# Kernel tuning notes

Measured on AMD Instinct MI355X. Metric: run time of the kernel, lower is better.

The kernel has to match this reference:

```python
import jax, jax.numpy as jnp
from jax import lax
import numpy as np

B, L, D = 16, 512, 256
F, K = 256, 3
M = 2048
EPS = 1e-5


def setup_inputs() -> dict:
    key = jax.random.key(0)
    ks = jax.random.split(key, 12)
    x = jax.random.normal(ks[0], (B, L, D), jnp.float32)
    # integer durations >= 1, sum over L <= 3*512 = 1536 < M, as in training targets
    target = jax.random.randint(ks[1], (B, L), 1, 4)
    s = 0.02
    conv1_w = jax.random.normal(ks[2], (F, D, K), jnp.float32) * s
    conv1_b = jnp.zeros((F,), jnp.float32)
    ln1_g = jnp.ones((F,), jnp.float32)
    ln1_b = jnp.zeros((F,), jnp.float32)
    conv2_w = jax.random.normal(ks[3], (F, F, K), jnp.float32) * s
    conv2_b = jnp.zeros((F,), jnp.float32)
    ln2_g = jnp.ones((F,), jnp.float32)
    ln2_b = jnp.zeros((F,), jnp.float32)
    lin_w = jax.random.normal(ks[4], (F, 1), jnp.float32) * s
    lin_b = jnp.zeros((1,), jnp.float32)
    return dict(x=x, target=target, mel_max_length=M,
                conv1_w=conv1_w, conv1_b=conv1_b, ln1_g=ln1_g, ln1_b=ln1_b,
                conv2_w=conv2_w, conv2_b=conv2_b, ln2_g=ln2_g, ln2_b=ln2_b,
                lin_w=lin_w, lin_b=lin_b)


def _layer_norm(h, g, b):
    mu = jnp.mean(h, axis=-1, keepdims=True)
    var = jnp.mean(jnp.square(h - mu), axis=-1, keepdims=True)
    return (h - mu) * lax.rsqrt(var + EPS) * g + b


def _conv1d(h_bld, w, b):
    # h: (B, L, C_in), w: (C_out, C_in, K) -> (B, L, C_out), SAME padding
    pad = (w.shape[-1] - 1) // 2
    h = jnp.transpose(h_bld, (0, 2, 1))  # (B, C, L)
    h = lax.conv_general_dilated(h, w, (1,), [(pad, pad)],
                                 dimension_numbers=('NCH', 'OIH', 'NCH'))
    return jnp.transpose(h + b[None, :, None], (0, 2, 1))


def _duration_predictor(x, conv1_w, conv1_b, ln1_g, ln1_b,
                        conv2_w, conv2_b, ln2_g, ln2_b, lin_w, lin_b):
    # FastSpeech duration predictor (eval mode: dropout = identity)
    h = jax.nn.relu(_layer_norm(_conv1d(x, conv1_w, conv1_b), ln1_g, ln1_b))
    h = jax.nn.relu(_layer_norm(_conv1d(h, conv2_w, conv2_b), ln2_g, ln2_b))
    return jax.nn.relu(h @ lin_w + lin_b)[..., 0]  # (B, L)


def _length_regulate(x, dur, mel_max_length):
    # alignment[b,m,l] = 1 iff cs[l-1] <= m < cs[l]  (exactly the scatter+diff trick
    # of create_alignment, padded to mel_max_length as in the original F.pad)
    cs = jnp.cumsum(dur, axis=1)              # (B, L) inclusive cumsum
    prev = cs - dur                           # exclusive cumsum
    m = jnp.arange(mel_max_length)[None, :, None]  # (1, M, 1)
    align = ((m >= prev[:, None, :]) & (m < cs[:, None, :])).astype(x.dtype)  # (B,M,L)
    return jnp.einsum('bml,bld->bmd', align, x)


def reference(x, target, mel_max_length, conv1_w, conv1_b, ln1_g, ln1_b,
              conv2_w, conv2_b, ln2_g, ln2_b, lin_w, lin_b):
    dup = _duration_predictor(x, conv1_w, conv1_b, ln1_g, ln1_b,
                              conv2_w, conv2_b, ln2_g, ln2_b, lin_w, lin_b)
    output = _length_regulate(x, target, mel_max_length)
    return (output, dup)
```

## Files before the change

### kernel.cpp

```cpp
#include <hip/hip_runtime.h>
#include <hip/hip_bf16.h>

#define Bn 16
#define Ln 512
#define Cn 256
#define Fn 256
#define Kn 3
#define Mn 2048

#define NKSTEP 24
#define MT 32
#define XS_PS 264
#define NCONVBLK 256

typedef __attribute__((ext_vector_type(8))) short short8;
typedef __attribute__((ext_vector_type(4))) float f32x4;

static __device__ __forceinline__ unsigned short f2bf(float f) {
    unsigned int u = __float_as_uint(f);
    return (unsigned short)((u + 0x7fff + ((u >> 16) & 1)) >> 16);
}

__global__ __launch_bounds__(256) void pack_scan(
    const float* __restrict__ w1, const float* __restrict__ w2,
    unsigned short* __restrict__ bp1, unsigned short* __restrict__ bp2,
    const int* __restrict__ target, int* __restrict__ map)
{
    __shared__ int ss[256];
    const int blk = blockIdx.x;
    const int t = threadIdx.x;
    if (blk < 1536) {
        int i = blk * 256 + t;
        const float* w = w1;
        unsigned short* bp = bp1;
        if (i >= Fn * Cn * Kn) { i -= Fn * Cn * Kn; w = w2; bp = bp2; }
        int j    = i & 7;
        int lane = (i >> 3) & 63;
        int nt   = (i >> 9) & 15;
        int s    = i >> 13;
        int kap = s * 32 + ((lane >> 4) * 8) + j;
        int k = kap >> 8;
        int d = kap & 255;
        int f = nt * 16 + (lane & 15);
        bp[i] = f2bf(w[(f * Cn + d) * Kn + k]);
    } else {
        int b = blk - 1536;
        int v0 = target[b * Ln + 2 * t];
        int v1 = target[b * Ln + 2 * t + 1];
        ss[t] = v0 + v1;
        __syncthreads();
        for (int off = 1; off < 256; off <<= 1) {
            int add = (t >= off) ? ss[t - off] : 0;
            __syncthreads();
            ss[t] += add;
            __syncthreads();
        }
        int S     = ss[t];
        int total = ss[255];
        int cs1   = S;
        int cs0   = S - v1;
        int prev0 = cs0 - v0;
        for (int m = prev0; m < cs0; ++m) map[b * Mn + m] = 2 * t;
        for (int m = cs0;   m < cs1; ++m) map[b * Mn + m] = 2 * t + 1;
        for (int m = total + t; m < Mn; m += 256) map[b * Mn + m] = -1;
    }
}

template <bool IS_F32_IN, bool DO_LINEAR, bool WITH_REG>
__global__ __launch_bounds__(256) void conv_mfma(
    const void* __restrict__ in_,
    const unsigned short* __restrict__ bp,
    const float* __restrict__ bias,
    const float* __restrict__ gamma,
    const float* __restrict__ beta,
    const float* __restrict__ lw,
    const float* __restrict__ lb,
    unsigned short* __restrict__ hout,
    float* __restrict__ dup,
    const float* __restrict__ gx,
    const int* __restrict__ gmap,
    float* __restrict__ gout)
{
    __shared__ __align__(16) unsigned short xs[(MT + 2) * XS_PS];
    __shared__ float2 red[MT][4];
    __shared__ float  red2[MT][4];

    const int t = threadIdx.x;

    if (WITH_REG && blockIdx.x >= NCONVBLK) {
        int e4 = (blockIdx.x - NCONVBLK) * 256 + t;
        int d4 = e4 & 63;
        int bm = e4 >> 6;
        int b  = bm >> 11;
        int l  = gmap[bm];
        float4 val = make_float4(0.f, 0.f, 0.f, 0.f);
        if (l >= 0) val = *((const float4*)(gx + (size_t)(b * Ln + l) * Cn) + d4);
        ((float4*)gout)[e4] = val;
        return;
    }

    const int b  = blockIdx.x >> 4;
    const int l0 = (blockIdx.x & 15) * MT;

    if (IS_F32_IN) {
        const float* in = (const float*)in_;
        for (int idx = t; idx < (MT + 2) * 64; idx += 256) {
            int row = idx >> 6;
            int c4  = (idx & 63) * 4;
            int l = l0 + row - 1;
            float4 v = make_float4(0.f, 0.f, 0.f, 0.f);
            if (l >= 0 && l < Ln) v = *(const float4*)&in[((size_t)b * Ln + l) * Cn + c4];
            unsigned int lo = (unsigned int)f2bf(v.x) | ((unsigned int)f2bf(v.y) << 16);
            unsigned int hi = (unsigned int)f2bf(v.z) | ((unsigned int)f2bf(v.w) << 16);
            *(uint2*)&xs[row * XS_PS + c4] = make_uint2(lo, hi);
        }
    } else {
        const unsigned short* in = (const unsigned short*)in_;
        for (int idx = t; idx < (MT + 2) * 32; idx += 256) {
            int row = idx >> 5;
            int c8  = (idx & 31) * 8;
            int l = l0 + row - 1;
            uint4 v = make_uint4(0u, 0u, 0u, 0u);
            if (l >= 0 && l < Ln) v = *(const uint4*)&in[((size_t)b * Ln + l) * Cn + c8];
            *(uint4*)&xs[row * XS_PS + c8] = v;
        }
    }
    __syncthreads();

    const int lane = t & 63;
    const int wv   = t >> 6;
    const int mrow = lane & 15;
    const int q    = lane >> 4;

    f32x4  acc[2][4] = {};
    short8 bfr[2][4];
    short8 afr[2][2];

    auto loadB = [&](int s, int slot) {
        const unsigned short* p = bp + (size_t)((s * 16 + wv * 4) * 64 + lane) * 8;
        #pragma unroll
        for (int i = 0; i < 4; ++i)
            bfr[slot][i] = *(const short8*)(p + (size_t)i * 64 * 8);
    };
    auto loadA = [&](int s, int slot) {
        const int k    = s >> 3;
        const int dcol = (s & 7) * 32 + q * 8;
        #pragma unroll
        for (int mt = 0; mt < 2; ++mt)
            afr[slot][mt] = *(const short8*)&xs[(mt * 16 + mrow + k) * XS_PS + dcol];
    };

    loadB(0, 0); loadA(0, 0);
    loadB(1, 1); loadA(1, 1);

    #pragma unroll 2
    for (int s = 0; s < NKSTEP; ++s) {
        const int slot = s & 1;
        #pragma unroll
        for (int mt = 0; mt < 2; ++mt)
            #pragma unroll
            for (int i = 0; i < 4; ++i)
                acc[mt][i] = __builtin_amdgcn_mfma_f32_16x16x32_bf16(
                    afr[slot][mt], bfr[slot][i], acc[mt][i], 0, 0, 0);
        const int sn = (s + 2 < NKSTEP) ? (s + 2) : s;
        loadB(sn, slot);
        loadA(sn, slot);
    }

    float gv[4], bv[4], lwv[4], biasv[4];
    #pragma unroll
    for (int i = 0; i < 4; ++i) {
        int col = wv * 64 + i * 16 + mrow;
        biasv[i] = bias[col];
        gv[i]    = gamma[col];
        bv[i]    = beta[col];
        if (DO_LINEAR) lwv[i] = lw[col];
    }
    #pragma unroll
    for (int mt = 0; mt < 2; ++mt)
        #pragma unroll
        for (int i = 0; i < 4; ++i)
            #pragma unroll
            for (int r = 0; r < 4; ++r)
                acc[mt][i][r] += biasv[i];

    #pragma unroll
    for (int mt = 0; mt < 2; ++mt)
        #pragma unroll
        for (int r = 0; r < 4; ++r) {
            float s  = acc[mt][0][r] + acc[mt][1][r] + acc[mt][2][r] + acc[mt][3][r];
            float sq = acc[mt][0][r] * acc[mt][0][r] + acc[mt][1][r] * acc[mt][1][r]
                     + acc[mt][2][r] * acc[mt][2][r] + acc[mt][3][r] * acc[mt][3][r];
            #pragma unroll
            for (int off = 1; off <= 8; off <<= 1) {
                s  += __shfl_xor(s,  off, 64);
                sq += __shfl_xor(sq, off, 64);
            }
            if (mrow == 0) red[mt * 16 + q * 4 + r][wv] = make_float2(s, sq);
        }
    __syncthreads();

    float muv[2][4], rsv[2][4];
    #pragma unroll
    for (int mt = 0; mt < 2; ++mt)
        #pragma unroll
        for (int r = 0; r < 4; ++r) {
            int row = mt * 16 + q * 4 + r;
            float2 p0 = red[row][0], p1 = red[row][1], p2 = red[row][2], p3 = red[row][3];
            float s  = p0.x + p1.x + p2.x + p3.x;
            float sq = p0.y + p1.y + p2.y + p3.y;
            float mu  = s * (1.f / 256.f);
            float var = sq * (1.f / 256.f) - mu * mu;
            muv[mt][r] = mu;
            rsv[mt][r] = rsqrtf(var + 1e-5f);
        }

    if (!DO_LINEAR) {
        #pragma unroll
        for (int mt = 0; mt < 2; ++mt)
            #pragma unroll
            for (int r = 0; r < 4; ++r) {
                int l = l0 + mt * 16 + q * 4 + r;
                size_t base = ((size_t)b * Ln + l) * Fn;
                #pragma unroll
                for (int i = 0; i < 4; ++i) {
                    float o = fmaxf((acc[mt][i][r] - muv[mt][r]) * rsv[mt][r] * gv[i] + bv[i], 0.f);
                    hout[base + wv * 64 + i * 16 + mrow] = f2bf(o);
                }
            }
    } else {
        #pragma unroll
        for (int mt = 0; mt < 2; ++mt)
            #pragma unroll
            for (int r = 0; r < 4; ++r) {
                float dot = 0.f;
                #pragma unroll
                for (int i = 0; i < 4; ++i) {
                    float o = fmaxf((acc[mt][i][r] - muv[mt][r]) * rsv[mt][r] * gv[i] + bv[i], 0.f);
                    dot += o * lwv[i];
                }
                #pragma unroll
                for (int off = 1; off <= 8; off <<= 1)
                    dot += __shfl_xor(dot, off, 64);
                if (mrow == 0) red2[mt * 16 + q * 4 + r][wv] = dot;
            }
        __syncthreads();
        if (t < MT) {
            float d = red2[t][0] + red2[t][1] + red2[t][2] + red2[t][3];
            dup[b * Ln + l0 + t] = fmaxf(d + lb[0], 0.f);
        }
    }
}

extern "C" void kernel_launch(void* const* d_in, const int* in_sizes, int n_in,
                              void* d_out, int out_size, void* d_ws, size_t ws_size,
                              hipStream_t stream) {
    const float* x    = (const float*)d_in[0];
    const int*   targ = (const int*)d_in[1];
    const float* c1w = (const float*)d_in[3];
    const float* c1b = (const float*)d_in[4];
    const float* g1  = (const float*)d_in[5];
    const float* be1 = (const float*)d_in[6];
    const float* c2w = (const float*)d_in[7];
    const float* c2b = (const float*)d_in[8];
    const float* g2  = (const float*)d_in[9];
    const float* be2 = (const float*)d_in[10];
    const float* lw  = (const float*)d_in[11];
    const float* lb  = (const float*)d_in[12];

    float* out     = (float*)d_out;
    float* out_dup = out + (size_t)Bn * Mn * Cn;

    char* ws = (char*)d_ws;
    unsigned short* bp1 = (unsigned short*)ws;
    unsigned short* bp2 = (unsigned short*)(ws + 393216);
    unsigned short* h1  = (unsigned short*)(ws + 2 * 393216);
    int*            map = (int*)(ws + 2 * 393216 + 4194304);

    pack_scan<<<1552, 256, 0, stream>>>(c1w, c2w, bp1, bp2, targ, map);

    conv_mfma<true, false, true><<<NCONVBLK + (Bn * Mn * Cn / 4) / 256, 256, 0, stream>>>(
        (const void*)x, bp1, c1b, g1, be1, nullptr, nullptr, h1, nullptr,
        x, map, out);

    conv_mfma<false, true, false><<<NCONVBLK, 256, 0, stream>>>(
        (const void*)h1, bp2, c2b, g2, be2, lw, lb, nullptr, out_dup,
        nullptr, nullptr, nullptr);
}
```

Measured before the change: 117.8 us.

## Retile conv to 64-row tiles with 512 threads and move conv2 weight packing into gather kernel

Measured after the change: 141.9 us. 1.2x slower.

```diff
diff --git a/kernel.cpp b/kernel.cpp
--- a/kernel.cpp
+++ b/kernel.cpp
@@ -9,9 +9,11 @@
 #define Mn 2048
 
 #define NKSTEP 24
-#define MT 32
+#define MT 64
 #define XS_PS 264
-#define NCONVBLK 256
+#define NCONV 128
+#define NGATH 1024
+#define NPACK 384
 
 typedef __attribute__((ext_vector_type(8))) short short8;
 typedef __attribute__((ext_vector_type(4))) float f32x4;
@@ -21,53 +23,47 @@
     return (unsigned short)((u + 0x7fff + ((u >> 16) & 1)) >> 16);
 }
 
-__global__ __launch_bounds__(256) void pack_scan(
-    const float* __restrict__ w1, const float* __restrict__ w2,
-    unsigned short* __restrict__ bp1, unsigned short* __restrict__ bp2,
+static __device__ __forceinline__ void pack_one(const float* __restrict__ w,
+                                                unsigned short* __restrict__ bp,
+                                                int i) {
+    int j    = i & 7;
+    int lane = (i >> 3) & 63;
+    int nt   = (i >> 9) & 15;
+    int s    = i >> 13;
+    int kap = s * 32 + ((lane >> 4) * 8) + j;
+    int k = kap >> 8;
+    int d = kap & 255;
+    int f = nt * 16 + (lane & 15);
+    bp[i] = f2bf(w[(f * Cn + d) * Kn + k]);
+}
+
+__global__ __launch_bounds__(512) void pack_scan(
+    const float* __restrict__ w1, unsigned short* __restrict__ bp1,
     const int* __restrict__ target, int* __restrict__ map)
 {
-    __shared__ int ss[256];
+    __shared__ int ss[Ln];
     const int blk = blockIdx.x;
     const int t = threadIdx.x;
-    if (blk < 1536) {
-        int i = blk * 256 + t;
-        const float* w = w1;
-        unsigned short* bp = bp1;
-        if (i >= Fn * Cn * Kn) { i -= Fn * Cn * Kn; w = w2; bp = bp2; }
-        int j    = i & 7;
-        int lane = (i >> 3) & 63;
-        int nt   = (i >> 9) & 15;
-        int s    = i >> 13;
-        int kap = s * 32 + ((lane >> 4) * 8) + j;
-        int k = kap >> 8;
-        int d = kap & 255;
-        int f = nt * 16 + (lane & 15);
-        bp[i] = f2bf(w[(f * Cn + d) * Kn + k]);
-    } else {
-        int b = blk - 1536;
-        int v0 = target[b * Ln + 2 * t];
-        int v1 = target[b * Ln + 2 * t + 1];
-        ss[t] = v0 + v1;
+    if (blk < NPACK) { pack_one(w1, bp1, blk * 512 + t); return; }
+    int b = blk - NPACK;
+    int v = target[b * Ln + t];
+    ss[t] = v;
+    __syncthreads();
+    for (int off = 1; off < Ln; off <<= 1) {
+        int add = (t >= off) ? ss[t - off] : 0;
         __syncthreads();
-        for (int off = 1; off < 256; off <<= 1) {
-            int add = (t >= off) ? ss[t - off] : 0;
-            __syncthreads();
-            ss[t] += add;
-            __syncthreads();
-        }
-        int S     = ss[t];
-        int total = ss[255];
-        int cs1   = S;
-        int cs0   = S - v1;
-        int prev0 = cs0 - v0;
-        for (int m = prev0; m < cs0; ++m) map[b * Mn + m] = 2 * t;
-        for (int m = cs0;   m < cs1; ++m) map[b * Mn + m] = 2 * t + 1;
-        for (int m = total + t; m < Mn; m += 256) map[b * Mn + m] = -1;
-    }
-}
-
-template <bool IS_F32_IN, bool DO_LINEAR, bool WITH_REG>
-__global__ __launch_bounds__(256) void conv_mfma(
+        ss[t] += add;
+        __syncthreads();
+    }
+    int cs    = ss[t];
+    int prev  = cs - v;
+    int total = ss[Ln - 1];
+    for (int m = prev; m < cs; ++m) map[b * Mn + m] = t;
+    for (int m = total + t; m < Mn; m += Ln) map[b * Mn + m] = -1;
+}
+
+template <bool IS_F32_IN, bool DO_LINEAR, bool WITH_AUX>
+__global__ __launch_bounds__(512) void conv_mfma(
     const void* __restrict__ in_,
     const unsigned short* __restrict__ bp,
     const float* __restrict__ bias,
@@ -79,32 +75,41 @@
     float* __restrict__ dup,
     const float* __restrict__ gx,
     const int* __restrict__ gmap,
-    float* __restrict__ gout)
+    float* __restrict__ gout,
+    const float* __restrict__ wsrc,
+    unsigned short* __restrict__ bpdst)
 {
     __shared__ __align__(16) unsigned short xs[(MT + 2) * XS_PS];
-    __shared__ float2 red[MT][4];
-    __shared__ float  red2[MT][4];
+    __shared__ float2 red[MT][8];
+    __shared__ float  red2[MT][8];
 
     const int t = threadIdx.x;
 
-    if (WITH_REG && blockIdx.x >= NCONVBLK) {
-        int e4 = (blockIdx.x - NCONVBLK) * 256 + t;
-        int d4 = e4 & 63;
-        int bm = e4 >> 6;
-        int b  = bm >> 11;
-        int l  = gmap[bm];
-        float4 val = make_float4(0.f, 0.f, 0.f, 0.f);
-        if (l >= 0) val = *((const float4*)(gx + (size_t)(b * Ln + l) * Cn) + d4);
-        ((float4*)gout)[e4] = val;
+    if (WITH_AUX && blockIdx.x >= NCONV) {
+        int rel = blockIdx.x - NCONV;
+        if (rel < NGATH) {
+            int bm = rel * 32 + (t >> 4);
+            int l  = gmap[bm];
+            int b  = bm >> 11;
+            int lc = (l >= 0) ? l : 0;
+            const float4* src = (const float4*)(gx + ((size_t)b * Ln + lc) * Cn) + (t & 15);
+            float4* dst = (float4*)gout + (size_t)bm * 64 + (t & 15);
+            float4 z = make_float4(0.f, 0.f, 0.f, 0.f);
+            #pragma unroll
+            for (int j = 0; j < 4; ++j)
+                dst[j * 16] = (l >= 0) ? src[j * 16] : z;
+        } else {
+            pack_one(wsrc, bpdst, (rel - NGATH) * 512 + t);
+        }
         return;
     }
 
-    const int b  = blockIdx.x >> 4;
-    const int l0 = (blockIdx.x & 15) * MT;
+    const int b  = blockIdx.x >> 3;
+    const int l0 = (blockIdx.x & 7) * MT;
 
     if (IS_F32_IN) {
         const float* in = (const float*)in_;
-        for (int idx = t; idx < (MT + 2) * 64; idx += 256) {
+        for (int idx = t; idx < (MT + 2) * 64; idx += 512) {
             int row = idx >> 6;
             int c4  = (idx & 63) * 4;
             int l = l0 + row - 1;
@@ -116,7 +121,7 @@
         }
     } else {
         const unsigned short* in = (const unsigned short*)in_;
-        for (int idx = t; idx < (MT + 2) * 32; idx += 256) {
+        for (int idx = t; idx < (MT + 2) * 32; idx += 512) {
             int row = idx >> 5;
             int c8  = (idx & 31) * 8;
             int l = l0 + row - 1;
@@ -132,65 +137,62 @@
     const int mrow = lane & 15;
     const int q    = lane >> 4;
 
-    f32x4  acc[2][4] = {};
-    short8 bfr[2][4];
-    short8 afr[2][2];
+    f32x4  acc[4][2] = {};
+    short8 bfr[3][2];
+    short8 afr[3][4];
 
     auto loadB = [&](int s, int slot) {
-        const unsigned short* p = bp + (size_t)((s * 16 + wv * 4) * 64 + lane) * 8;
-        #pragma unroll
-        for (int i = 0; i < 4; ++i)
-            bfr[slot][i] = *(const short8*)(p + (size_t)i * 64 * 8);
+        const unsigned short* p = bp + (size_t)((s * 16 + wv * 2) * 64 + lane) * 8;
+        bfr[slot][0] = *(const short8*)p;
+        bfr[slot][1] = *(const short8*)(p + 512);
     };
     auto loadA = [&](int s, int slot) {
         const int k    = s >> 3;
         const int dcol = (s & 7) * 32 + q * 8;
         #pragma unroll
-        for (int mt = 0; mt < 2; ++mt)
+        for (int mt = 0; mt < 4; ++mt)
             afr[slot][mt] = *(const short8*)&xs[(mt * 16 + mrow + k) * XS_PS + dcol];
     };
 
     loadB(0, 0); loadA(0, 0);
     loadB(1, 1); loadA(1, 1);
-
-    #pragma unroll 2
+    loadB(2, 2); loadA(2, 2);
+
+    #pragma unroll
     for (int s = 0; s < NKSTEP; ++s) {
-        const int slot = s & 1;
-        #pragma unroll
-        for (int mt = 0; mt < 2; ++mt)
-            #pragma unroll
-            for (int i = 0; i < 4; ++i)
+        const int slot = s % 3;
+        #pragma unroll
+        for (int mt = 0; mt < 4; ++mt)
+            #pragma unroll
+            for (int i = 0; i < 2; ++i)
                 acc[mt][i] = __builtin_amdgcn_mfma_f32_16x16x32_bf16(
                     afr[slot][mt], bfr[slot][i], acc[mt][i], 0, 0, 0);
-        const int sn = (s + 2 < NKSTEP) ? (s + 2) : s;
-        loadB(sn, slot);
-        loadA(sn, slot);
-    }
-
-    float gv[4], bv[4], lwv[4], biasv[4];
-    #pragma unroll
-    for (int i = 0; i < 4; ++i) {
-        int col = wv * 64 + i * 16 + mrow;
+        if (s + 3 < NKSTEP) { loadB(s + 3, slot); loadA(s + 3, slot); }
+    }
+
+    float biasv[2], gv[2], bv[2], lwv[2];
+    #pragma unroll
+    for (int i = 0; i < 2; ++i) {
+        int col = wv * 32 + i * 16 + mrow;
         biasv[i] = bias[col];
         gv[i]    = gamma[col];
         bv[i]    = beta[col];
         if (DO_LINEAR) lwv[i] = lw[col];
     }
     #pragma unroll
-    for (int mt = 0; mt < 2; ++mt)
-        #pragma unroll
-        for (int i = 0; i < 4; ++i)
+    for (int mt = 0; mt < 4; ++mt)
+        #pragma unroll
+        for (int i = 0; i < 2; ++i)
             #pragma unroll
             for (int r = 0; r < 4; ++r)
                 acc[mt][i][r] += biasv[i];
 
     #pragma unroll
-    for (int mt = 0; mt < 2; ++mt)
+    for (int mt = 0; mt < 4; ++mt)
         #pragma unroll
         for (int r = 0; r < 4; ++r) {
-            float s  = acc[mt][0][r] + acc[mt][1][r] + acc[mt][2][r] + acc[mt][3][r];
-            float sq = acc[mt][0][r] * acc[mt][0][r] + acc[mt][1][r] * acc[mt][1][r]
-                     + acc[mt][2][r] * acc[mt][2][r] + acc[mt][3][r] * acc[mt][3][r];
+            float s  = acc[mt][0][r] + acc[mt][1][r];
+            float sq = acc[mt][0][r] * acc[mt][0][r] + acc[mt][1][r] * acc[mt][1][r];
             #pragma unroll
             for (int off = 1; off <= 8; off <<= 1) {
                 s  += __shfl_xor(s,  off, 64);
@@ -200,15 +202,18 @@
         }
     __syncthreads();
 
-    float muv[2][4], rsv[2][4];
-    #pragma unroll
-    for (int mt = 0; mt < 2; ++mt)
+    float muv[4][4], rsv[4][4];
+    #pragma unroll
+    for (int mt = 0; mt < 4; ++mt)
         #pragma unroll
         for (int r = 0; r < 4; ++r) {
             int row = mt * 16 + q * 4 + r;
-            float2 p0 = red[row][0], p1 = red[row][1], p2 = red[row][2], p3 = red[row][3];
-            float s  = p0.x + p1.x + p2.x + p3.x;
-            float sq = p0.y + p1.y + p2.y + p3.y;
+            float s = 0.f, sq = 0.f;
+            #pragma unroll
+            for (int w = 0; w < 8; ++w) {
+                float2 p = red[row][w];
+                s += p.x; sq += p.y;
+            }
             float mu  = s * (1.f / 256.f);
             float var = sq * (1.f / 256.f) - mu * mu;
             muv[mt][r] = mu;
@@ -217,25 +222,25 @@
 
     if (!DO_LINEAR) {
         #pragma unroll
-        for (int mt = 0; mt < 2; ++mt)
+        for (int mt = 0; mt < 4; ++mt)
             #pragma unroll
             for (int r = 0; r < 4; ++r) {
                 int l = l0 + mt * 16 + q * 4 + r;
                 size_t base = ((size_t)b * Ln + l) * Fn;
                 #pragma unroll
-                for (int i = 0; i < 4; ++i) {
+                for (int i = 0; i < 2; ++i) {
                     float o = fmaxf((acc[mt][i][r] - muv[mt][r]) * rsv[mt][r] * gv[i] + bv[i], 0.f);
-                    hout[base + wv * 64 + i * 16 + mrow] = f2bf(o);
+                    hout[base + wv * 32 + i * 16 + mrow] = f2bf(o);
                 }
             }
     } else {
         #pragma unroll
-        for (int mt = 0; mt < 2; ++mt)
+        for (int mt = 0; mt < 4; ++mt)
             #pragma unroll
             for (int r = 0; r < 4; ++r) {
                 float dot = 0.f;
                 #pragma unroll
-                for (int i = 0; i < 4; ++i) {
+                for (int i = 0; i < 2; ++i) {
                     float o = fmaxf((acc[mt][i][r] - muv[mt][r]) * rsv[mt][r] * gv[i] + bv[i], 0.f);
                     dot += o * lwv[i];
                 }
@@ -246,7 +251,9 @@
             }
         __syncthreads();
         if (t < MT) {
-            float d = red2[t][0] + red2[t][1] + red2[t][2] + red2[t][3];
+            float d = 0.f;
+            #pragma unroll
+            for (int w = 0; w < 8; ++w) d += red2[t][w];
             dup[b * Ln + l0 + t] = fmaxf(d + lb[0], 0.f);
         }
     }
@@ -277,13 +284,13 @@
     unsigned short* h1  = (unsigned short*)(ws + 2 * 393216);
     int*            map = (int*)(ws + 2 * 393216 + 4194304);
 
-    pack_scan<<<1552, 256, 0, stream>>>(c1w, c2w, bp1, bp2, targ, map);
-
-    conv_mfma<true, false, true><<<NCONVBLK + (Bn * Mn * Cn / 4) / 256, 256, 0, stream>>>(
+    pack_scan<<<NPACK + Bn, 512, 0, stream>>>(c1w, bp1, targ, map);
+
+    conv_mfma<true, false, true><<<NCONV + NGATH + NPACK, 512, 0, stream>>>(
         (const void*)x, bp1, c1b, g1, be1, nullptr, nullptr, h1, nullptr,
-        x, map, out);
-
-    conv_mfma<false, true, false><<<NCONVBLK, 256, 0, stream>>>(
+        x, map, out, c2w, bp2);
+
+    conv_mfma<false, true, false><<<NCONV, 512, 0, stream>>>(
         (const void*)h1, bp2, c2b, g2, be2, lw, lb, nullptr, out_dup,
-        nullptr, nullptr, nullptr);
-}
+        nullptr, nullptr, nullptr, nullptr, nullptr);
+}
```
